# Kernel optimization log

Measured on AMD Instinct MI355X. Metric: run time of the kernel, lower is better.

The kernel has to match this reference:

```python
import jax, jax.numpy as jnp
import numpy as np

B, V, D, R = 2, 4096, 192, 16
E, H = 2 * D, 8
DH = E // H
K, TK = 16, 8


def _ln(x, g, b):
    m = x.mean(-1, keepdims=True)
    v = ((x - m) ** 2).mean(-1, keepdims=True)
    return (x - m) * jax.lax.rsqrt(v + 1e-5) * g + b


def _coords():
    # voxel centers in [-1,1]^3, (V,3)
    r = (jnp.arange(R, dtype=jnp.float32) + 0.5) / R * 2.0 - 1.0
    return jnp.stack(jnp.meshgrid(r, r, r, indexing='ij'), -1).reshape(-1, 3)


def setup_inputs() -> dict:
    key = jax.random.key(0)
    ks = jax.random.split(key, 10)
    s = 0.02
    return {
        'voxel_tokens': jax.random.normal(ks[0], (B, V, D), jnp.float32),
        'non_empty_mask': jax.random.randint(ks[1], (B, V), 0, 2).astype(bool),
        'We': jax.random.normal(ks[2], (D, E)) * s, 'be': jnp.zeros((E,)),
        'g1': jnp.ones((E,)), 'bt1': jnp.zeros((E,)),
        'Wqkv': jax.random.normal(ks[3], (E, 3 * E)) * s, 'bqkv': jnp.zeros((3 * E,)),
        'Wo': jax.random.normal(ks[4], (E, E)) * s, 'bo': jnp.zeros((E,)),
        'Wc': jax.random.normal(ks[5], (E, D)) * s, 'bc': jnp.zeros((D,)),
        'g2': jnp.ones((E,)), 'bt2': jnp.zeros((E,)),
        'W1': jax.random.normal(ks[6], (E, 2 * E)) * s, 'b1': jnp.zeros((2 * E,)),
        'W2': jax.random.normal(ks[7], (2 * E, E)) * s, 'b2': jnp.zeros((E,)),
    }


def reference(voxel_tokens, non_empty_mask, We, be, g1, bt1, Wqkv, bqkv, Wo, bo,
              Wc, bc, g2, bt2, W1, b1, W2, b2):
    fmask = non_empty_mask.astype(voxel_tokens.dtype)  # (B,V)
    shortcut = voxel_tokens
    x = voxel_tokens @ We + be                          # expand: (B,V,E)
    x = _ln(x, g1, bt1)
    # --- sparse dynamic voxel attention ---
    c = _coords()
    d2 = jnp.sum((c[:, None, :] - c[None, :, :]) ** 2, -1)  # (V,V)
    big = jnp.asarray(1e9, x.dtype)
    dmask = d2[None] + (1.0 - fmask)[:, None, :] * big      # empty keys pushed away
    _, knn = jax.lax.top_k(-dmask, K)                        # (B,V,K) nearest non-empty
    qkv = x @ Wqkv + bqkv
    q, k, v = jnp.split(qkv, 3, axis=-1)                     # (B,V,E) each
    bidx = jnp.arange(B)[:, None, None]
    kn = k[bidx, knn].reshape(B, V, K, H, DH)                # gathered neighbor keys
    vn = v[bidx, knn].reshape(B, V, K, H, DH)
    qh = q.reshape(B, V, H, DH)
    scores = jnp.einsum('bvhd,bvkhd->bvhk', qh, kn) / jnp.sqrt(jnp.asarray(DH, x.dtype))
    nvalid = fmask[bidx, knn]                                # (B,V,K)
    scores = jnp.where(nvalid[:, :, None, :] > 0, scores, -big)
    sel, sidx = jax.lax.top_k(scores, TK)                    # top_k_select by score
    attn = jax.nn.softmax(sel, axis=-1)                      # (B,V,H,TK)
    vt = vn.transpose(0, 1, 3, 2, 4)                         # (B,V,H,K,DH)
    vsel = jnp.take_along_axis(vt, sidx[..., None], axis=3)  # (B,V,H,TK,DH)
    o = jnp.einsum('bvhk,bvhkd->bvhd', attn, vsel).reshape(B, V, E)
    o = o @ Wo + bo
    # masked scatter: empty voxels -> zeros (reconstruct_dense_masked_scatter_2)
    x = o * fmask[..., None]
    x = x @ Wc + bc                                          # contract
    x = x * 0.5 + shortcut                                   # DropPath(0) -> identity
    x2 = x @ We + be
    x2 = _ln(x2, g2, bt2)
    x2 = jax.nn.gelu(x2 @ W1 + b1) @ W2 + b2                 # FeedForward(E, 2E)
    x2 = x2 @ Wc + bc
    return x2 * 0.5 + x
```

## Files before the change

### kernel.cpp

```cpp
#include <hip/hip_runtime.h>
#include <stdint.h>


using u16 = unsigned short;
using u32 = unsigned int;
using u64 = unsigned long long;

typedef short short8 __attribute__((ext_vector_type(8)));
typedef float f32x4 __attribute__((ext_vector_type(4)));

#define DEV static __device__ __forceinline__

constexpr int cV = 4096, cD = 192;
constexpr int cE = 384;
constexpr int cKN = 16, cTK = 8;
constexpr int cM = 2 * cV;
constexpr int c3E = 1152;

DEV float bf2f(u16 v) { return __uint_as_float(((u32)v) << 16); }
DEV float bflo(u32 v) { return __uint_as_float(v << 16); }
DEV float bfhi(u32 v) { return __uint_as_float(v & 0xFFFF0000u); }
DEV u16 f2bf(float f) {
  u32 u = __float_as_uint(f);
  u = (u + 0x7FFFu + ((u >> 16) & 1u)) >> 16;
  return (u16)u;
}
DEV int mget(const void* mp, int flag, int i) {
  if (flag == 0) return ((const int*)mp)[i] != 0;
  if (flag == 1) return ((const float*)mp)[i] != 0.0f;
  if (flag == 2) return ((const u16*)mp)[i] != 0;
  return ((const unsigned char*)mp)[i] != 0;
}
DEV float gelu_tanh(float x) {
  float t = tanhf(0.7978845608028654f * (x + 0.044715f * x * x * x));
  return 0.5f * x * (1.0f + t);
}
DEV u32 f2ord(float f) {
  u32 u = __float_as_uint(f);
  return (u & 0x80000000u) ? ~u : (u | 0x80000000u);
}
DEV float ord2f(u32 o) {
  u32 bits = (o & 0x80000000u) ? (o & 0x7FFFFFFFu) : ~o;
  return __uint_as_float(bits);
}
DEV int bf_plausible(u32 h) {
  if (h == 0u || h == 0x8000u) return 1;
  u32 e = (h >> 7) & 0xFFu;
  return (e >= 100u && e <= 140u) ? 1 : 0;
}

using as1p = const unsigned int __attribute__((address_space(1)))*;
using as3p = unsigned int __attribute__((address_space(3)))*;
DEV void gload16(const void* g, void* l) {
  __builtin_amdgcn_global_load_lds((as1p)g, (as3p)l, 16, 0, 0);
}
DEV f32x4 mfma16x16x32_bf16(short8 a, short8 b, f32x4 c) {
  asm volatile("v_mfma_f32_16x16x32_bf16 %0, %1, %2, %0" : "+v"(c) : "v"(a), "v"(b));
  return c;
}
DEV int swz(int row, int byteoff) { return byteoff ^ ((row & 7) << 4); }
DEV int ldswz(int r, int c) { return r * 64 + (c ^ ((r & 7) * 8)); }
#define SBPIN() __builtin_amdgcn_sched_barrier(0)

struct BF { short8 v[3][2]; };
DEV void loadBF(BF& b, const u16* __restrict__ fbase, int nKB, int kb, int lane) {
  #pragma unroll
  for (int n = 0; n < 3; ++n)
    #pragma unroll
    for (int ks = 0; ks < 2; ++ks)
      b.v[n][ks] = *(const short8*)(fbase + ((size_t)n * nKB + kb + ks) * 512 + lane * 8);
}

template <int T, typename AF>
DEV void rstage_1x8(const u16* __restrict__ fbase, int nKB, int kb0,
                    int lane, int l15, int l4,
                    f32x4 (&acc)[2][3], AF&& aread) {
  BF bp[2];
  loadBF(bp[0], fbase, nKB, kb0, lane);
  #pragma unroll
  for (int t = 0; t < T; ++t) {
    if (t + 1 < T) loadBF(bp[(t + 1) & 1], fbase, nKB, kb0 + 2 * (t + 1), lane);
    #pragma unroll
    for (int ks = 0; ks < 2; ++ks) {
      short8 a0 = aread(0, t, ks);
      short8 a1 = aread(1, t, ks);
      #pragma unroll
      for (int n = 0; n < 3; ++n) {
        acc[0][n] = mfma16x16x32_bf16(a0, bp[t & 1].v[n][ks], acc[0][n]);
        acc[1][n] = mfma16x16x32_bf16(a1, bp[t & 1].v[n][ks], acc[1][n]);
      }
    }
  }
}

template <int T, typename AF>
DEV void rstage_2x4(const u16* __restrict__ fbase, int nKB, int kb0,
                    int lane, int l15, int l4,
                    f32x4 (&acc)[3], AF&& aread) {
  BF bp[2];
  loadBF(bp[0], fbase, nKB, kb0, lane);
  #pragma unroll
  for (int t = 0; t < T; ++t) {
    if (t + 1 < T) loadBF(bp[(t + 1) & 1], fbase, nKB, kb0 + 2 * (t + 1), lane);
    #pragma unroll
    for (int ks = 0; ks < 2; ++ks) {
      short8 a = aread(t, ks);
      #pragma unroll
      for (int n = 0; n < 3; ++n)
        acc[n] = mfma16x16x32_bf16(a, bp[t & 1].v[n][ks], acc[n]);
    }
  }
}

__global__ void detect_all_kernel(const u32* __restrict__ tok,
                                  const u32* __restrict__ m,
                                  int* __restrict__ flag) {
  __shared__ int cnt, sa, sb, sc;
  if (threadIdx.x == 0) { cnt = 0; sa = 0; sb = 0; sc = 0; }
  __syncthreads();
  int c = 0;
  for (int i = threadIdx.x; i < 4096; i += 256) {
    u32 d = tok[i];
    c += bf_plausible(d & 0xFFFFu) & bf_plausible(d >> 16);
  }
  atomicAdd(&cnt, c);
  int a = 0, b = 0, cc = 0;
  for (int i = threadIdx.x; i < 2048; i += 256) {
    u32 d = m[i];
    if (!(d == 0u || d == 1u)) a = 1;
    if (!(d == 0u || d == 0x3F800000u)) b = 1;
    if (!(d == 0u || d == 0x00003F80u || d == 0x3F800000u || d == 0x3F803F80u)) cc = 1;
  }
  if (a) atomicOr(&sa, 1);
  if (b) atomicOr(&sb, 1);
  if (cc) atomicOr(&sc, 1);
  __syncthreads();
  if (threadIdx.x == 0) {
    flag[1] = (cnt > 3400) ? 1 : 0;
    flag[0] = (sa == 0) ? 0 : ((sb == 0) ? 1 : ((sc == 0) ? 2 : 3));
  }
}

struct PrepArgs {
  const void* csrc[11]; u16* cdst[11]; int cn[11];
  const void* tsrc[6]; u16* tdst[6]; int tK[6]; int tN[6];
  const void* mask; u64* bm;
};
__global__ __launch_bounds__(256) void prep_kernel(PrepArgs a, const int* __restrict__ flag) {
  const int job = blockIdx.y;
  const int dt = flag[1];
  if (job < 11) {
    const int n = a.cn[job];
    u16* d = a.cdst[job];
    if (dt) {
      const u16* s = (const u16*)a.csrc[job];
      for (int i = blockIdx.x * 256 + threadIdx.x; i < n; i += gridDim.x * 256) d[i] = s[i];
    } else {
      const float* s = (const float*)a.csrc[job];
      for (int i = blockIdx.x * 256 + threadIdx.x; i < n; i += gridDim.x * 256) d[i] = f2bf(s[i]);
    }
  } else if (job < 17) {
    const int t = job - 11;
    const int K = a.tK[t], N = a.tN[t];
    const int nKB = K >> 5;
    const int total = K * N;
    u16* d = a.tdst[t];
    for (int i = blockIdx.x * 256 + threadIdx.x; i < total; i += gridDim.x * 256) {
      const int frag = i >> 9;
      const int r = i & 511;
      const int lane = r >> 3, e = r & 7;
      const int l4 = lane >> 4, l15 = lane & 15;
      const int colblk = frag / nKB;
      const int kblk = frag - colblk * nKB;
      const int n = colblk * 16 + l15;
      const int k = kblk * 32 + l4 * 8 + e;
      u16 vv;
      if (dt) vv = ((const u16*)a.tsrc[t])[(size_t)k * N + n];
      else vv = f2bf(((const float*)a.tsrc[t])[(size_t)k * N + n]);
      d[i] = vv;
    }
  } else {
    const int gw = (blockIdx.x * 256 + threadIdx.x) >> 6;
    const int lane = threadIdx.x & 63;
    if (gw < 128) {
      const int fl = flag[0];
      u64 bal = __ballot(mget(a.mask, fl, gw * 64 + lane) != 0);
      if (lane == 0) a.bm[gw] = bal;
    }
  }
}

__global__ __launch_bounds__(256) void knn_kernel(const u64* __restrict__ bitmask,
                                                  int* __restrict__ knn_out) {
  const int tid = threadIdx.x;
  const int wid = tid >> 6, lane = tid & 63;
  const int q0 = blockIdx.x * 4;
  const int b = q0 >> 12;
  const int q = q0 + wid;
  const int v = q & 4095;
  __shared__ u64 smask[64];
  __shared__ int hist4[4][64];
  __shared__ int listT[4][64];
  __shared__ int out16s[4][16];
  __shared__ int meta[4][3];
  __shared__ int cntA[4], cntT[4];
  if (tid < 64) smask[tid] = bitmask[b * 64 + tid];
  for (int i = tid; i < 4 * 64; i += 256) ((int*)hist4)[i] = 0;
  if (lane == 0) { cntA[wid] = 0; cntT[wid] = 0; }
  __syncthreads();
  const int iv = v >> 8, jv = (v >> 4) & 15, kv = v & 15;
  #pragma unroll
  for (int t = 0; t < 12; ++t) {
    int o = t * 64 + lane;
    if (o < 729) {
      int oi = o / 81, rm = o - oi * 81;
      int oj = rm / 9, ok = rm - oj * 9;
      int i = iv + oi - 4, j = jv + oj - 4, k = kv + ok - 4;
      if (((i | j | k) & ~15) == 0) {
        int u = (i << 8) | (j << 4) | k;
        if ((smask[u >> 6] >> (u & 63)) & 1ull) {
          int di = oi - 4, dj = oj - 4, dk = ok - 4;
          atomicAdd(&hist4[wid][di * di + dj * dj + dk * dk], 1);
        }
      }
    }
  }
  __syncthreads();
  if (lane == 0) {
    int cum = 0, T = -1, below = 0;
    for (int d = 0; d <= 48; ++d) {
      int h = hist4[wid][d];
      if (h > 0 && cum + h >= cKN) { T = d; below = cum; break; }
      cum += h;
    }
    if (T > 24) T = -1;
    meta[wid][0] = T; meta[wid][1] = below; meta[wid][2] = (T < 0) ? 1 : 0;
  }
  __syncthreads();
  const int T = meta[wid][0], below = meta[wid][1], fb = meta[wid][2];
  #pragma unroll
  for (int t = 0; t < 12; ++t) {
    int o = t * 64 + lane;
    if (o < 729) {
      int oi = o / 81, rm = o - oi * 81;
      int oj = rm / 9, ok = rm - oj * 9;
      int i = iv + oi - 4, j = jv + oj - 4, k = kv + ok - 4;
      if (((i | j | k) & ~15) == 0) {
        int u = (i << 8) | (j << 4) | k;
        if ((smask[u >> 6] >> (u & 63)) & 1ull) {
          int di = oi - 4, dj = oj - 4, dk = ok - 4;
          int d2 = di * di + dj * dj + dk * dk;
          if (d2 < T) { int p = atomicAdd(&cntA[wid], 1); out16s[wid][p] = u; }
          else if (d2 == T) { int p = atomicAdd(&cntT[wid], 1); if (p < 64) listT[wid][p] = u; }
        }
      }
    }
  }
  __syncthreads();
  if (!fb) {
    if (lane == 0) {
      int need = cKN - below;
      int nT = cntT[wid] < 64 ? cntT[wid] : 64;
      for (int r = 0; r < need; ++r) {
        int bi = 0, bu = 0x7FFFFFFF;
        for (int i2 = 0; i2 < nT; ++i2) { int x = listT[wid][i2]; if (x < bu) { bu = x; bi = i2; } }
        out16s[wid][below + r] = bu;
        listT[wid][bi] = 0x7FFFFFFF;
      }
    }
  } else {
    u64 rem = smask[lane];
    const int myi = lane >> 2;
    const int di2 = (iv - myi) * (iv - myi);
    for (int r = 0; r < cKN; ++r) {
      u64 tmp = rem;
      u32 best = 0xFFFFFFFFu;
      while (tmp) {
        int bp = __builtin_ctzll(tmp);
        tmp &= tmp - 1;
        int u = (lane << 6) | bp;
        int dj = jv - ((u >> 4) & 15), dk = kv - (u & 15);
        u32 key = (u32)(((di2 + dj * dj + dk * dk) << 12) | u);
        if (key < best) best = key;
      }
      u32 pk = (best == 0xFFFFFFFFu) ? 0xFFFFFFFFu : ((best << 6) | (u32)lane);
      #pragma unroll
      for (int off = 1; off < 64; off <<= 1) {
        u32 o2 = __shfl_xor(pk, off);
        if (o2 < pk) pk = o2;
      }
      int u = (int)((pk >> 6) & 4095u);
      int wl = (int)(pk & 63u);
      if (lane == wl) rem &= ~(1ull << (u & 63));
      if (lane == 0) out16s[wid][r] = u;
    }
  }
  __syncthreads();
  if (lane < cKN) knn_out[q * cKN + lane] = out16s[wid][lane];
}

__global__ __launch_bounds__(512) void fused_ln_qkv(
    const u16* __restrict__ tokc, const u16* __restrict__ WeF,
    const u16* __restrict__ be, const u16* __restrict__ g1, const u16* __restrict__ bt1,
    const u16* __restrict__ WqkvF, const u16* __restrict__ bqkv,
    u16* __restrict__ QB) {
  __shared__ alignas(16) u16 Afull[3 * 2048];
  __shared__ alignas(16) char X1[32 * 768];
  __shared__ float st[32][8][2];
  const int tid = threadIdx.x;
  const int lane = tid & 63, wn = tid >> 6;
  const int l15 = lane & 15, l4 = lane >> 4;
  const int sr = lane >> 3;
  const int scs = (((lane & 7) ^ sr) << 3);
  const int row0 = blockIdx.x * 32;

  for (int g = wn; g < 12; g += 8)
    gload16(tokc + (size_t)(row0 + (g & 3) * 8 + sr) * 192 + (g >> 2) * 64 + scs,
            (char*)Afull + g * 1024);
  SBPIN();
  __syncthreads();

  f32x4 acc[2][3];
  #pragma unroll
  for (int m = 0; m < 2; ++m)
    #pragma unroll
    for (int n = 0; n < 3; ++n) acc[m][n] = f32x4{0.f, 0.f, 0.f, 0.f};
  rstage_1x8<3>(WeF + (size_t)(wn * 3) * 6 * 512, 6, 0, lane, l15, l4, acc,
                [&](int m, int t, int ks) {
                  return *(const short8*)&Afull[t * 2048 + ldswz(m * 16 + l15, ks * 32 + l4 * 8)];
                });
  float s[2][4], sq[2][4];
  #pragma unroll
  for (int m = 0; m < 2; ++m)
    #pragma unroll
    for (int j = 0; j < 4; ++j) { s[m][j] = 0.f; sq[m][j] = 0.f; }
  #pragma unroll
  for (int n = 0; n < 3; ++n) {
    const float bi = bf2f(be[wn * 48 + n * 16 + l15]);
    #pragma unroll
    for (int m = 0; m < 2; ++m)
      #pragma unroll
      for (int j = 0; j < 4; ++j) {
        acc[m][n][j] += bi;
        s[m][j] += acc[m][n][j]; sq[m][j] += acc[m][n][j] * acc[m][n][j];
      }
  }
  #pragma unroll
  for (int off = 1; off < 16; off <<= 1)
    #pragma unroll
    for (int m = 0; m < 2; ++m)
      #pragma unroll
      for (int j = 0; j < 4; ++j) { s[m][j] += __shfl_xor(s[m][j], off); sq[m][j] += __shfl_xor(sq[m][j], off); }
  if (l15 == 0) {
    #pragma unroll
    for (int m = 0; m < 2; ++m)
      #pragma unroll
      for (int j = 0; j < 4; ++j) {
        const int rl = m * 16 + l4 * 4 + j;
        st[rl][wn][0] = s[m][j]; st[rl][wn][1] = sq[m][j];
      }
  }
  __syncthreads();
  #pragma unroll
  for (int m = 0; m < 2; ++m)
    #pragma unroll
    for (int j = 0; j < 4; ++j) {
      const int rl = m * 16 + l4 * 4 + j;
      float ts = 0.f, tq = 0.f;
      #pragma unroll
      for (int wv = 0; wv < 8; ++wv) { ts += st[rl][wv][0]; tq += st[rl][wv][1]; }
      const float mean = ts * (1.0f / 384.0f);
      const float var = tq * (1.0f / 384.0f) - mean * mean;
      const float rstd = rsqrtf(var + 1e-5f);
      #pragma unroll
      for (int n = 0; n < 3; ++n) {
        const int col = wn * 48 + n * 16 + l15;
        const float v = (acc[m][n][j] - mean) * rstd * bf2f(g1[col]) + bf2f(bt1[col]);
        *(u16*)(X1 + swz(rl, rl * 768 + col * 2)) = f2bf(v);
      }
    }
  __syncthreads();

  for (int chunk = 0; chunk < 3; ++chunk) {
    f32x4 a2[2][3];
    #pragma unroll
    for (int m = 0; m < 2; ++m)
      #pragma unroll
      for (int n = 0; n < 3; ++n) a2[m][n] = f32x4{0.f, 0.f, 0.f, 0.f};
    rstage_1x8<6>(WqkvF + (size_t)(chunk * 24 + wn * 3) * 12 * 512, 12, 0, lane, l15, l4, a2,
                  [&](int m, int t, int ks) {
                    const int rl = m * 16 + l15;
                    return *(const short8*)(X1 + swz(rl, rl * 768 + (t * 64 + ks * 32 + l4 * 8) * 2));
                  });
    #pragma unroll
    for (int n = 0; n < 3; ++n) {
      const int col = chunk * 384 + wn * 48 + n * 16 + l15;
      const float bi = bf2f(bqkv[col]);
      #pragma unroll
      for (int m = 0; m < 2; ++m)
        #pragma unroll
        for (int j = 0; j < 4; ++j)
          QB[(size_t)(row0 + m * 16 + l4 * 4 + j) * c3E + col] = f2bf(a2[m][n][j] + bi);
    }
  }
}

__global__ __launch_bounds__(512) void fused_cd(
    const u16* __restrict__ S2, const u16* __restrict__ WoF, const u16* __restrict__ bo,
    const void* __restrict__ mask, const int* __restrict__ flag,
    const u16* __restrict__ WcF, const u16* __restrict__ bc, const u16* __restrict__ tokc,
    const u16* __restrict__ WeF, const u16* __restrict__ be,
    const u16* __restrict__ g2, const u16* __restrict__ bt2,
    const u16* __restrict__ W1F, const u16* __restrict__ b1,
    const u16* __restrict__ W2F, const u16* __restrict__ b2,
    void* __restrict__ outv) {
  __shared__ alignas(16) u16 Afull[6 * 2048];
  __shared__ alignas(16) char Tb[32 * 768];
  __shared__ float st[32][8][2];
  char* HbA = (char*)Afull;
  const int tid = threadIdx.x;
  const int lane = tid & 63, wn = tid >> 6;
  const int wr = wn >> 2, wc = wn & 3;
  const int l15 = lane & 15, l4 = lane >> 4;
  const int sr = lane >> 3;
  const int scs = (((lane & 7) ^ sr) << 3);
  const int row0 = blockIdx.x * 32;
  const int fl = flag[0];

  for (int g = wn; g < 24; g += 8)
    gload16(S2 + (size_t)(row0 + (g & 3) * 8 + sr) * cE + (g >> 2) * 64 + scs,
            (char*)Afull + g * 1024);
  SBPIN();
  __syncthreads();

  {
    f32x4 acc[2][3];
    #pragma unroll
    for (int m = 0; m < 2; ++m)
      #pragma unroll
      for (int n = 0; n < 3; ++n) acc[m][n] = f32x4{0.f, 0.f, 0.f, 0.f};
    rstage_1x8<6>(WoF + (size_t)(wn * 3) * 12 * 512, 12, 0, lane, l15, l4, acc,
                  [&](int m, int t, int ks) {
                    return *(const short8*)&Afull[t * 2048 + ldswz(m * 16 + l15, ks * 32 + l4 * 8)];
                  });
    #pragma unroll
    for (int m = 0; m < 2; ++m)
      #pragma unroll
      for (int j = 0; j < 4; ++j) {
        const int rl = m * 16 + l4 * 4 + j;
        const float fm = mget(mask, fl, row0 + rl) ? 1.0f : 0.0f;
        #pragma unroll
        for (int n = 0; n < 3; ++n) {
          const int col = wn * 48 + n * 16 + l15;
          const float v = (acc[m][n][j] + bf2f(bo[col])) * fm;
          *(u16*)(Tb + swz(rl, rl * 768 + col * 2)) = f2bf(v);
        }
      }
  }
  __syncthreads();

  f32x4 xm[3];
  #pragma unroll
  for (int n = 0; n < 3; ++n) xm[n] = f32x4{0.f, 0.f, 0.f, 0.f};
  rstage_2x4<6>(WcF + (size_t)(wc * 3) * 12 * 512, 12, 0, lane, l15, l4, xm,
                [&](int t, int ks) {
                  const int rl = wr * 16 + l15;
                  return *(const short8*)(Tb + swz(rl, rl * 768 + (t * 64 + ks * 32 + l4 * 8) * 2));
                });
  __syncthreads();
  #pragma unroll
  for (int n = 0; n < 3; ++n) {
    const int col = wc * 48 + n * 16 + l15;
    const float bi = bf2f(bc[col]);
    #pragma unroll
    for (int j = 0; j < 4; ++j) {
      const int rl = wr * 16 + l4 * 4 + j;
      xm[n][j] = (xm[n][j] + bi) * 0.5f + bf2f(tokc[(size_t)(row0 + rl) * cD + col]);
      *(u16*)(Tb + swz(rl, rl * 384 + col * 2)) = f2bf(xm[n][j]);
    }
  }
  __syncthreads();

  {
    f32x4 a3[2][3];
    #pragma unroll
    for (int m = 0; m < 2; ++m)
      #pragma unroll
      for (int n = 0; n < 3; ++n) a3[m][n] = f32x4{0.f, 0.f, 0.f, 0.f};
    rstage_1x8<3>(WeF + (size_t)(wn * 3) * 6 * 512, 6, 0, lane, l15, l4, a3,
                  [&](int m, int t, int ks) {
                    const int rl = m * 16 + l15;
                    return *(const short8*)(Tb + swz(rl, rl * 384 + (t * 64 + ks * 32 + l4 * 8) * 2));
                  });
    float s[2][4], sq[2][4];
    #pragma unroll
    for (int m = 0; m < 2; ++m)
      #pragma unroll
      for (int j = 0; j < 4; ++j) { s[m][j] = 0.f; sq[m][j] = 0.f; }
    #pragma unroll
    for (int n = 0; n < 3; ++n) {
      const float bi = bf2f(be[wn * 48 + n * 16 + l15]);
      #pragma unroll
      for (int m = 0; m < 2; ++m)
        #pragma unroll
        for (int j = 0; j < 4; ++j) {
          a3[m][n][j] += bi;
          s[m][j] += a3[m][n][j]; sq[m][j] += a3[m][n][j] * a3[m][n][j];
        }
    }
    #pragma unroll
    for (int off = 1; off < 16; off <<= 1)
      #pragma unroll
      for (int m = 0; m < 2; ++m)
        #pragma unroll
        for (int j = 0; j < 4; ++j) { s[m][j] += __shfl_xor(s[m][j], off); sq[m][j] += __shfl_xor(sq[m][j], off); }
    if (l15 == 0) {
      #pragma unroll
      for (int m = 0; m < 2; ++m)
        #pragma unroll
        for (int j = 0; j < 4; ++j) {
          const int rl = m * 16 + l4 * 4 + j;
          st[rl][wn][0] = s[m][j]; st[rl][wn][1] = sq[m][j];
        }
    }
    __syncthreads();
    #pragma unroll
    for (int m = 0; m < 2; ++m)
      #pragma unroll
      for (int j = 0; j < 4; ++j) {
        const int rl = m * 16 + l4 * 4 + j;
        float ts = 0.f, tq = 0.f;
        #pragma unroll
        for (int wv = 0; wv < 8; ++wv) { ts += st[rl][wv][0]; tq += st[rl][wv][1]; }
        const float mean = ts * (1.0f / 384.0f);
        const float var = tq * (1.0f / 384.0f) - mean * mean;
        const float rstd = rsqrtf(var + 1e-5f);
        #pragma unroll
        for (int n = 0; n < 3; ++n) {
          const int col = wn * 48 + n * 16 + l15;
          const float v = (a3[m][n][j] - mean) * rstd * bf2f(g2[col]) + bf2f(bt2[col]);
          *(u16*)(Tb + swz(rl, rl * 768 + col * 2)) = f2bf(v);
        }
      }
  }
  __syncthreads();

  f32x4 accF[2][3];
  #pragma unroll
  for (int m = 0; m < 2; ++m)
    #pragma unroll
    for (int n = 0; n < 3; ++n) accF[m][n] = f32x4{0.f, 0.f, 0.f, 0.f};

  for (int half = 0; half < 2; ++half) {
    {
      f32x4 a1[2][3];
      #pragma unroll
      for (int m = 0; m < 2; ++m)
        #pragma unroll
        for (int n = 0; n < 3; ++n) a1[m][n] = f32x4{0.f, 0.f, 0.f, 0.f};
      rstage_1x8<6>(W1F + (size_t)(half * 24 + wn * 3) * 12 * 512, 12, 0, lane, l15, l4, a1,
                    [&](int m, int t, int ks) {
                      const int rl = m * 16 + l15;
                      return *(const short8*)(Tb + swz(rl, rl * 768 + (t * 64 + ks * 32 + l4 * 8) * 2));
                    });
      #pragma unroll
      for (int n = 0; n < 3; ++n) {
        const int col = wn * 48 + n * 16 + l15;
        const float bi = bf2f(b1[half * 384 + col]);
        #pragma unroll
        for (int m = 0; m < 2; ++m)
          #pragma unroll
          for (int j = 0; j < 4; ++j) {
            const int rl = m * 16 + l4 * 4 + j;
            *(u16*)(HbA + swz(rl, rl * 768 + col * 2)) = f2bf(gelu_tanh(a1[m][n][j] + bi));
          }
      }
    }
    __syncthreads();
    rstage_1x8<6>(W2F + (size_t)(wn * 3) * 24 * 512, 24, half * 12, lane, l15, l4, accF,
                  [&](int m, int t, int ks) {
                    const int rl = m * 16 + l15;
                    return *(const short8*)(HbA + swz(rl, rl * 768 + (t * 64 + ks * 32 + l4 * 8) * 2));
                  });
    __syncthreads();
  }
  #pragma unroll
  for (int n = 0; n < 3; ++n) {
    const int col = wn * 48 + n * 16 + l15;
    const float bi = bf2f(b2[col]);
    #pragma unroll
    for (int m = 0; m < 2; ++m)
      #pragma unroll
      for (int j = 0; j < 4; ++j) {
        const int rl = m * 16 + l4 * 4 + j;
        *(u16*)(HbA + swz(rl, rl * 768 + col * 2)) = f2bf(accF[m][n][j] + bi);
      }
  }
  __syncthreads();
  f32x4 a3[3];
  #pragma unroll
  for (int n = 0; n < 3; ++n) a3[n] = f32x4{0.f, 0.f, 0.f, 0.f};
  rstage_2x4<6>(WcF + (size_t)(wc * 3) * 12 * 512, 12, 0, lane, l15, l4, a3,
                [&](int t, int ks) {
                  const int rl = wr * 16 + l15;
                  return *(const short8*)(HbA + swz(rl, rl * 768 + (t * 64 + ks * 32 + l4 * 8) * 2));
                });
  u16* o16 = (u16*)outv;
  float* o32 = (float*)outv;
  const int dtf = flag[1];
  #pragma unroll
  for (int n = 0; n < 3; ++n) {
    const int col = wc * 48 + n * 16 + l15;
    const float bi = bf2f(bc[col]);
    #pragma unroll
    for (int j = 0; j < 4; ++j) {
      const int rl = wr * 16 + l4 * 4 + j;
      const size_t oi = (size_t)(row0 + rl) * cD + col;
      const float r = (a3[n][j] + bi) * 0.5f + xm[n][j];
      if (dtf) o16[oi] = f2bf(r);
      else o32[oi] = r;
    }
  }
}

__global__ __launch_bounds__(256) void attn_kernel(const u16* __restrict__ qkv,
                                                   const int* __restrict__ knn,
                                                   u16* __restrict__ o_out) {
  const int wid = threadIdx.x >> 6;
  const int lane = threadIdx.x & 63;
  const int bq = blockIdx.x * 4 + wid;
  const int b = bq >> 12;
  __shared__ float w4[4][8][8];
  __shared__ int vid4[4][8][8];
  __shared__ int nb4[4][16];
  float (*w)[8] = w4[wid];
  int (*vid)[8] = vid4[wid];
  int* nb = nb4[wid];
  if (lane < 16) nb[lane] = knn[bq * cKN + lane];
  const int h = lane >> 3;
  const int j = lane & 7;
  const uint2* qp = (const uint2*)(qkv + (size_t)bq * c3E + h * 48);
  const int r0 = nb[j], r1 = nb[j + 8];
  const uint2* k0p = (const uint2*)(qkv + ((size_t)(b * cV + r0)) * c3E + cE + h * 48);
  const uint2* k1p = (const uint2*)(qkv + ((size_t)(b * cV + r1)) * c3E + cE + h * 48);
  float s0 = 0.f, s1 = 0.f;
  #pragma unroll
  for (int t = 0; t < 12; ++t) {
    uint2 qv = qp[t];
    uint2 k0 = k0p[t];
    uint2 k1 = k1p[t];
    s0 += bflo(qv.x) * bflo(k0.x) + bfhi(qv.x) * bfhi(k0.x)
        + bflo(qv.y) * bflo(k0.y) + bfhi(qv.y) * bfhi(k0.y);
    s1 += bflo(qv.x) * bflo(k1.x) + bfhi(qv.x) * bfhi(k1.x)
        + bflo(qv.y) * bflo(k1.y) + bfhi(qv.y) * bfhi(k1.y);
  }
  const float inv = 0.14433756729740643f;
  u64 key0 = (((u64)f2ord(s0 * inv)) << 4) | (u64)(15 - j);
  u64 key1 = (((u64)f2ord(s1 * inv)) << 4) | (u64)(15 - (j + 8));
  float m0 = 0.f, Z = 0.f, myw = 0.f;
  int myv = 0;
  #pragma unroll
  for (int r = 0; r < cTK; ++r) {
    u64 best = key0 > key1 ? key0 : key1;
    u64 o1 = __shfl_xor(best, 1); if (o1 > best) best = o1;
    u64 o2 = __shfl_xor(best, 2); if (o2 > best) best = o2;
    u64 o4 = __shfl_xor(best, 4); if (o4 > best) best = o4;
    if (key0 == best) key0 = 0;
    if (key1 == best) key1 = 0;
    float sv = ord2f((u32)(best >> 4));
    int nsel = 15 - (int)(best & 15ull);
    if (r == 0) m0 = sv;
    float e = expf(sv - m0);
    Z += e;
    if (j == r) { myw = e; myv = nsel; }
  }
  w[h][j] = myw / Z;
  vid[h][j] = nb[myv];
  const u16* vbase = qkv + (size_t)(b * cV) * c3E + 2 * cE;
  #pragma unroll
  for (int rep = 0; rep < 6; ++rep) {
    int e = rep * 64 + lane;
    int h2 = e / 48;
    float acc = 0.f;
    #pragma unroll
    for (int t = 0; t < cTK; ++t)
      acc += w[h2][t] * bf2f(vbase[(size_t)vid[h2][t] * c3E + e]);
    o_out[(size_t)bq * cE + e] = f2bf(acc);
  }
}

extern "C" void kernel_launch(void* const* d_in, const int* in_sizes, int n_in,
                              void* d_out, int out_size, void* d_ws, size_t ws_size,
                              hipStream_t stream) {
  if (n_in < 18) return;
  const void* mask = d_in[1];

  char* ws = (char*)d_ws;
  size_t off = 0;
  auto alloc = [&](size_t bytes) { size_t o = off; off += (bytes + 255) & ~(size_t)255; return o; };
  int* flag  = (int*)(ws + alloc(256));
  u64* bmask = (u64*)(ws + alloc(128 * 8));
  int* knn   = (int*)(ws + alloc((size_t)cM * cKN * 4));
  u16* S2    = (u16*)(ws + alloc((size_t)cM * cE * 2));
  u16* QB    = (u16*)(ws + alloc((size_t)cM * c3E * 2));
  u16* tokc  = (u16*)(ws + alloc((size_t)cM * cD * 2));
  u16* be    = (u16*)(ws + alloc(cE * 2));
  u16* g1    = (u16*)(ws + alloc(cE * 2));
  u16* bt1   = (u16*)(ws + alloc(cE * 2));
  u16* bqkv  = (u16*)(ws + alloc(c3E * 2));
  u16* bo    = (u16*)(ws + alloc(cE * 2));
  u16* bc    = (u16*)(ws + alloc(cD * 2));
  u16* g2    = (u16*)(ws + alloc(cE * 2));
  u16* bt2   = (u16*)(ws + alloc(cE * 2));
  u16* b1    = (u16*)(ws + alloc(2 * cE * 2));
  u16* b2    = (u16*)(ws + alloc(cE * 2));
  u16* WeF   = (u16*)(ws + alloc((size_t)192 * 384 * 2));
  u16* WqkvF = (u16*)(ws + alloc((size_t)384 * 1152 * 2));
  u16* WoF   = (u16*)(ws + alloc((size_t)384 * 384 * 2));
  u16* WcF   = (u16*)(ws + alloc((size_t)384 * 192 * 2));
  u16* W1F   = (u16*)(ws + alloc((size_t)384 * 768 * 2));
  u16* W2F   = (u16*)(ws + alloc((size_t)768 * 384 * 2));
  (void)ws_size; (void)in_sizes; (void)out_size;

  detect_all_kernel<<<1, 256, 0, stream>>>((const u32*)d_in[0], (const u32*)mask, flag);

  {
    PrepArgs pa;
    const int csrci[11] = {0, 3, 4, 5, 7, 9, 11, 12, 13, 15, 17};
    u16* cdsts[11] = {tokc, be, g1, bt1, bqkv, bo, bc, g2, bt2, b1, b2};
    const int cns[11] = {cM * cD, cE, cE, cE, c3E, cE, cD, cE, cE, 2 * cE, cE};
    for (int i = 0; i < 11; ++i) { pa.csrc[i] = d_in[csrci[i]]; pa.cdst[i] = cdsts[i]; pa.cn[i] = cns[i]; }
    const int tsrci[6] = {2, 6, 8, 10, 14, 16};
    u16* tdsts[6] = {WeF, WqkvF, WoF, WcF, W1F, W2F};
    const int tKs[6] = {192, 384, 384, 384, 384, 768};
    const int tNs[6] = {384, 1152, 384, 192, 768, 384};
    for (int i = 0; i < 6; ++i) { pa.tsrc[i] = d_in[tsrci[i]]; pa.tdst[i] = tdsts[i]; pa.tK[i] = tKs[i]; pa.tN[i] = tNs[i]; }
    pa.mask = mask; pa.bm = bmask;
    prep_kernel<<<dim3(96, 18), 256, 0, stream>>>(pa, flag);
  }

  knn_kernel<<<cM / 4, 256, 0, stream>>>(bmask, knn);

  const int GB = cM / 32;
  fused_ln_qkv<<<GB, 512, 0, stream>>>(tokc, WeF, be, g1, bt1, WqkvF, bqkv, QB);
  attn_kernel<<<cM / 4, 256, 0, stream>>>(QB, knn, S2);
  fused_cd<<<GB, 512, 0, stream>>>(S2, WoF, bo, mask, flag, WcF, bc, tokc,
                                   WeF, be, g2, bt2, W1F, b1, W2F, b2, d_out);
}
```

Baseline: 140.7 us.

## Halve row tile of fused GEMM kernels to 16 rows for more blocks

The fused LN+QKV and contract/FFN kernels now process 16 rows per block instead of 32, doubling the grid to 512 blocks and cutting shared memory per block. The goal is better occupancy and more parallelism across the GPU's compute units for a small M. In exchange, every block re-streams the full weight matrices from global/L2, so weight traffic per output row doubles. Half the waves sit idle during the 192-column Wc stages.

```diff
diff --git a/kernel.cpp b/kernel.cpp
--- a/kernel.cpp
+++ b/kernel.cpp
@@ -72,31 +72,8 @@
 }
 
 template <int T, typename AF>
-DEV void rstage_1x8(const u16* __restrict__ fbase, int nKB, int kb0,
-                    int lane, int l15, int l4,
-                    f32x4 (&acc)[2][3], AF&& aread) {
-  BF bp[2];
-  loadBF(bp[0], fbase, nKB, kb0, lane);
-  #pragma unroll
-  for (int t = 0; t < T; ++t) {
-    if (t + 1 < T) loadBF(bp[(t + 1) & 1], fbase, nKB, kb0 + 2 * (t + 1), lane);
-    #pragma unroll
-    for (int ks = 0; ks < 2; ++ks) {
-      short8 a0 = aread(0, t, ks);
-      short8 a1 = aread(1, t, ks);
-      #pragma unroll
-      for (int n = 0; n < 3; ++n) {
-        acc[0][n] = mfma16x16x32_bf16(a0, bp[t & 1].v[n][ks], acc[0][n]);
-        acc[1][n] = mfma16x16x32_bf16(a1, bp[t & 1].v[n][ks], acc[1][n]);
-      }
-    }
-  }
-}
-
-template <int T, typename AF>
-DEV void rstage_2x4(const u16* __restrict__ fbase, int nKB, int kb0,
-                    int lane, int l15, int l4,
-                    f32x4 (&acc)[3], AF&& aread) {
+DEV void rstage(const u16* __restrict__ fbase, int nKB, int kb0,
+                int lane, f32x4 (&acc)[3], AF&& aread) {
   BF bp[2];
   loadBF(bp[0], fbase, nKB, kb0, lane);
   #pragma unroll
@@ -304,103 +281,84 @@
     const u16* __restrict__ be, const u16* __restrict__ g1, const u16* __restrict__ bt1,
     const u16* __restrict__ WqkvF, const u16* __restrict__ bqkv,
     u16* __restrict__ QB) {
-  __shared__ alignas(16) u16 Afull[3 * 2048];
-  __shared__ alignas(16) char X1[32 * 768];
-  __shared__ float st[32][8][2];
+  __shared__ alignas(16) u16 Afull[3 * 1024];
+  __shared__ alignas(16) char X1[16 * 768];
+  __shared__ float st[16][8][2];
   const int tid = threadIdx.x;
   const int lane = tid & 63, wn = tid >> 6;
   const int l15 = lane & 15, l4 = lane >> 4;
   const int sr = lane >> 3;
   const int scs = (((lane & 7) ^ sr) << 3);
-  const int row0 = blockIdx.x * 32;
-
-  for (int g = wn; g < 12; g += 8)
-    gload16(tokc + (size_t)(row0 + (g & 3) * 8 + sr) * 192 + (g >> 2) * 64 + scs,
+  const int row0 = blockIdx.x * 16;
+
+  for (int g = wn; g < 6; g += 8)
+    gload16(tokc + (size_t)(row0 + (g & 1) * 8 + sr) * 192 + (g >> 1) * 64 + scs,
             (char*)Afull + g * 1024);
   SBPIN();
   __syncthreads();
 
-  f32x4 acc[2][3];
-  #pragma unroll
-  for (int m = 0; m < 2; ++m)
-    #pragma unroll
-    for (int n = 0; n < 3; ++n) acc[m][n] = f32x4{0.f, 0.f, 0.f, 0.f};
-  rstage_1x8<3>(WeF + (size_t)(wn * 3) * 6 * 512, 6, 0, lane, l15, l4, acc,
-                [&](int m, int t, int ks) {
-                  return *(const short8*)&Afull[t * 2048 + ldswz(m * 16 + l15, ks * 32 + l4 * 8)];
-                });
-  float s[2][4], sq[2][4];
-  #pragma unroll
-  for (int m = 0; m < 2; ++m)
-    #pragma unroll
-    for (int j = 0; j < 4; ++j) { s[m][j] = 0.f; sq[m][j] = 0.f; }
+  f32x4 acc[3];
+  #pragma unroll
+  for (int n = 0; n < 3; ++n) acc[n] = f32x4{0.f, 0.f, 0.f, 0.f};
+  rstage<3>(WeF + (size_t)(wn * 3) * 6 * 512, 6, 0, lane, acc,
+            [&](int t, int ks) {
+              return *(const short8*)&Afull[t * 1024 + ldswz(l15, ks * 32 + l4 * 8)];
+            });
+  float s[4] = {0, 0, 0, 0}, sq[4] = {0, 0, 0, 0};
   #pragma unroll
   for (int n = 0; n < 3; ++n) {
     const float bi = bf2f(be[wn * 48 + n * 16 + l15]);
     #pragma unroll
-    for (int m = 0; m < 2; ++m)
-      #pragma unroll
-      for (int j = 0; j < 4; ++j) {
-        acc[m][n][j] += bi;
-        s[m][j] += acc[m][n][j]; sq[m][j] += acc[m][n][j] * acc[m][n][j];
-      }
+    for (int j = 0; j < 4; ++j) {
+      acc[n][j] += bi;
+      s[j] += acc[n][j]; sq[j] += acc[n][j] * acc[n][j];
+    }
   }
   #pragma unroll
   for (int off = 1; off < 16; off <<= 1)
     #pragma unroll
-    for (int m = 0; m < 2; ++m)
-      #pragma unroll
-      for (int j = 0; j < 4; ++j) { s[m][j] += __shfl_xor(s[m][j], off); sq[m][j] += __shfl_xor(sq[m][j], off); }
+    for (int j = 0; j < 4; ++j) { s[j] += __shfl_xor(s[j], off); sq[j] += __shfl_xor(sq[j], off); }
   if (l15 == 0) {
     #pragma unroll
-    for (int m = 0; m < 2; ++m)
-      #pragma unroll
-      for (int j = 0; j < 4; ++j) {
-        const int rl = m * 16 + l4 * 4 + j;
-        st[rl][wn][0] = s[m][j]; st[rl][wn][1] = sq[m][j];
-      }
-  }
-  __syncthreads();
-  #pragma unroll
-  for (int m = 0; m < 2; ++m)
-    #pragma unroll
     for (int j = 0; j < 4; ++j) {
-      const int rl = m * 16 + l4 * 4 + j;
-      float ts = 0.f, tq = 0.f;
-      #pragma unroll
-      for (int wv = 0; wv < 8; ++wv) { ts += st[rl][wv][0]; tq += st[rl][wv][1]; }
-      const float mean = ts * (1.0f / 384.0f);
-      const float var = tq * (1.0f / 384.0f) - mean * mean;
-      const float rstd = rsqrtf(var + 1e-5f);
-      #pragma unroll
-      for (int n = 0; n < 3; ++n) {
-        const int col = wn * 48 + n * 16 + l15;
-        const float v = (acc[m][n][j] - mean) * rstd * bf2f(g1[col]) + bf2f(bt1[col]);
-        *(u16*)(X1 + swz(rl, rl * 768 + col * 2)) = f2bf(v);
-      }
-    }
+      const int rl = l4 * 4 + j;
+      st[rl][wn][0] = s[j]; st[rl][wn][1] = sq[j];
+    }
+  }
+  __syncthreads();
+  #pragma unroll
+  for (int j = 0; j < 4; ++j) {
+    const int rl = l4 * 4 + j;
+    float ts = 0.f, tq = 0.f;
+    #pragma unroll
+    for (int wv = 0; wv < 8; ++wv) { ts += st[rl][wv][0]; tq += st[rl][wv][1]; }
+    const float mean = ts * (1.0f / 384.0f);
+    const float var = tq * (1.0f / 384.0f) - mean * mean;
+    const float rstd = rsqrtf(var + 1e-5f);
+    #pragma unroll
+    for (int n = 0; n < 3; ++n) {
+      const int col = wn * 48 + n * 16 + l15;
+      const float v = (acc[n][j] - mean) * rstd * bf2f(g1[col]) + bf2f(bt1[col]);
+      *(u16*)(X1 + swz(rl, rl * 768 + col * 2)) = f2bf(v);
+    }
+  }
   __syncthreads();
 
   for (int chunk = 0; chunk < 3; ++chunk) {
-    f32x4 a2[2][3];
-    #pragma unroll
-    for (int m = 0; m < 2; ++m)
-      #pragma unroll
-      for (int n = 0; n < 3; ++n) a2[m][n] = f32x4{0.f, 0.f, 0.f, 0.f};
-    rstage_1x8<6>(WqkvF + (size_t)(chunk * 24 + wn * 3) * 12 * 512, 12, 0, lane, l15, l4, a2,
-                  [&](int m, int t, int ks) {
-                    const int rl = m * 16 + l15;
-                    return *(const short8*)(X1 + swz(rl, rl * 768 + (t * 64 + ks * 32 + l4 * 8) * 2));
-                  });
+    f32x4 a2[3];
+    #pragma unroll
+    for (int n = 0; n < 3; ++n) a2[n] = f32x4{0.f, 0.f, 0.f, 0.f};
+    rstage<6>(WqkvF + (size_t)(chunk * 24 + wn * 3) * 12 * 512, 12, 0, lane, a2,
+              [&](int t, int ks) {
+                return *(const short8*)(X1 + swz(l15, l15 * 768 + (t * 64 + ks * 32 + l4 * 8) * 2));
+              });
     #pragma unroll
     for (int n = 0; n < 3; ++n) {
       const int col = chunk * 384 + wn * 48 + n * 16 + l15;
       const float bi = bf2f(bqkv[col]);
       #pragma unroll
-      for (int m = 0; m < 2; ++m)
-        #pragma unroll
-        for (int j = 0; j < 4; ++j)
-          QB[(size_t)(row0 + m * 16 + l4 * 4 + j) * c3E + col] = f2bf(a2[m][n][j] + bi);
+      for (int j = 0; j < 4; ++j)
+        QB[(size_t)(row0 + l4 * 4 + j) * c3E + col] = f2bf(a2[n][j] + bi);
     }
   }
 }
@@ -414,174 +372,150 @@
     const u16* __restrict__ W1F, const u16* __restrict__ b1,
     const u16* __restrict__ W2F, const u16* __restrict__ b2,
     void* __restrict__ outv) {
-  __shared__ alignas(16) u16 Afull[6 * 2048];
-  __shared__ alignas(16) char Tb[32 * 768];
-  __shared__ float st[32][8][2];
+  __shared__ alignas(16) u16 Afull[6 * 1024];
+  __shared__ alignas(16) char Tb[16 * 768];
+  __shared__ float st[16][8][2];
   char* HbA = (char*)Afull;
   const int tid = threadIdx.x;
   const int lane = tid & 63, wn = tid >> 6;
-  const int wr = wn >> 2, wc = wn & 3;
+  const int wc = wn & 3;
   const int l15 = lane & 15, l4 = lane >> 4;
   const int sr = lane >> 3;
   const int scs = (((lane & 7) ^ sr) << 3);
-  const int row0 = blockIdx.x * 32;
+  const int row0 = blockIdx.x * 16;
   const int fl = flag[0];
 
-  for (int g = wn; g < 24; g += 8)
-    gload16(S2 + (size_t)(row0 + (g & 3) * 8 + sr) * cE + (g >> 2) * 64 + scs,
+  for (int g = wn; g < 12; g += 8)
+    gload16(S2 + (size_t)(row0 + (g & 1) * 8 + sr) * cE + (g >> 1) * 64 + scs,
             (char*)Afull + g * 1024);
   SBPIN();
   __syncthreads();
 
   {
-    f32x4 acc[2][3];
-    #pragma unroll
-    for (int m = 0; m < 2; ++m)
-      #pragma unroll
-      for (int n = 0; n < 3; ++n) acc[m][n] = f32x4{0.f, 0.f, 0.f, 0.f};
-    rstage_1x8<6>(WoF + (size_t)(wn * 3) * 12 * 512, 12, 0, lane, l15, l4, acc,
-                  [&](int m, int t, int ks) {
-                    return *(const short8*)&Afull[t * 2048 + ldswz(m * 16 + l15, ks * 32 + l4 * 8)];
-                  });
-    #pragma unroll
-    for (int m = 0; m < 2; ++m)
+    f32x4 acc[3];
+    #pragma unroll
+    for (int n = 0; n < 3; ++n) acc[n] = f32x4{0.f, 0.f, 0.f, 0.f};
+    rstage<6>(WoF + (size_t)(wn * 3) * 12 * 512, 12, 0, lane, acc,
+              [&](int t, int ks) {
+                return *(const short8*)&Afull[t * 1024 + ldswz(l15, ks * 32 + l4 * 8)];
+              });
+    #pragma unroll
+    for (int j = 0; j < 4; ++j) {
+      const int rl = l4 * 4 + j;
+      const float fm = mget(mask, fl, row0 + rl) ? 1.0f : 0.0f;
+      #pragma unroll
+      for (int n = 0; n < 3; ++n) {
+        const int col = wn * 48 + n * 16 + l15;
+        const float v = (acc[n][j] + bf2f(bo[col])) * fm;
+        *(u16*)(Tb + swz(rl, rl * 768 + col * 2)) = f2bf(v);
+      }
+    }
+  }
+  __syncthreads();
+
+  f32x4 xm[3];
+  #pragma unroll
+  for (int n = 0; n < 3; ++n) xm[n] = f32x4{0.f, 0.f, 0.f, 0.f};
+  if (wn < 4) {
+    rstage<6>(WcF + (size_t)(wc * 3) * 12 * 512, 12, 0, lane, xm,
+              [&](int t, int ks) {
+                return *(const short8*)(Tb + swz(l15, l15 * 768 + (t * 64 + ks * 32 + l4 * 8) * 2));
+              });
+  }
+  __syncthreads();
+  if (wn < 4) {
+    #pragma unroll
+    for (int n = 0; n < 3; ++n) {
+      const int col = wc * 48 + n * 16 + l15;
+      const float bi = bf2f(bc[col]);
       #pragma unroll
       for (int j = 0; j < 4; ++j) {
-        const int rl = m * 16 + l4 * 4 + j;
-        const float fm = mget(mask, fl, row0 + rl) ? 1.0f : 0.0f;
-        #pragma unroll
-        for (int n = 0; n < 3; ++n) {
-          const int col = wn * 48 + n * 16 + l15;
-          const float v = (acc[m][n][j] + bf2f(bo[col])) * fm;
-          *(u16*)(Tb + swz(rl, rl * 768 + col * 2)) = f2bf(v);
-        }
-      }
-  }
-  __syncthreads();
-
-  f32x4 xm[3];
-  #pragma unroll
-  for (int n = 0; n < 3; ++n) xm[n] = f32x4{0.f, 0.f, 0.f, 0.f};
-  rstage_2x4<6>(WcF + (size_t)(wc * 3) * 12 * 512, 12, 0, lane, l15, l4, xm,
-                [&](int t, int ks) {
-                  const int rl = wr * 16 + l15;
-                  return *(const short8*)(Tb + swz(rl, rl * 768 + (t * 64 + ks * 32 + l4 * 8) * 2));
-                });
-  __syncthreads();
-  #pragma unroll
-  for (int n = 0; n < 3; ++n) {
-    const int col = wc * 48 + n * 16 + l15;
-    const float bi = bf2f(bc[col]);
-    #pragma unroll
-    for (int j = 0; j < 4; ++j) {
-      const int rl = wr * 16 + l4 * 4 + j;
-      xm[n][j] = (xm[n][j] + bi) * 0.5f + bf2f(tokc[(size_t)(row0 + rl) * cD + col]);
-      *(u16*)(Tb + swz(rl, rl * 384 + col * 2)) = f2bf(xm[n][j]);
+        const int rl = l4 * 4 + j;
+        xm[n][j] = (xm[n][j] + bi) * 0.5f + bf2f(tokc[(size_t)(row0 + rl) * cD + col]);
+        *(u16*)(Tb + swz(rl, rl * 384 + col * 2)) = f2bf(xm[n][j]);
+      }
     }
   }
   __syncthreads();
 
   {
-    f32x4 a3[2][3];
-    #pragma unroll
-    for (int m = 0; m < 2; ++m)
-      #pragma unroll
-      for (int n = 0; n < 3; ++n) a3[m][n] = f32x4{0.f, 0.f, 0.f, 0.f};
-    rstage_1x8<3>(WeF + (size_t)(wn * 3) * 6 * 512, 6, 0, lane, l15, l4, a3,
-                  [&](int m, int t, int ks) {
-                    const int rl = m * 16 + l15;
-                    return *(const short8*)(Tb + swz(rl, rl * 384 + (t * 64 + ks * 32 + l4 * 8) * 2));
-                  });
-    float s[2][4], sq[2][4];
-    #pragma unroll
-    for (int m = 0; m < 2; ++m)
-      #pragma unroll
-      for (int j = 0; j < 4; ++j) { s[m][j] = 0.f; sq[m][j] = 0.f; }
+    f32x4 a3[3];
+    #pragma unroll
+    for (int n = 0; n < 3; ++n) a3[n] = f32x4{0.f, 0.f, 0.f, 0.f};
+    rstage<3>(WeF + (size_t)(wn * 3) * 6 * 512, 6, 0, lane, a3,
+              [&](int t, int ks) {
+                return *(const short8*)(Tb + swz(l15, l15 * 384 + (t * 64 + ks * 32 + l4 * 8) * 2));
+              });
+    float s[4] = {0, 0, 0, 0}, sq[4] = {0, 0, 0, 0};
     #pragma unroll
     for (int n = 0; n < 3; ++n) {
       const float bi = bf2f(be[wn * 48 + n * 16 + l15]);
       #pragma unroll
-      for (int m = 0; m < 2; ++m)
-        #pragma unroll
-        for (int j = 0; j < 4; ++j) {
-          a3[m][n][j] += bi;
-          s[m][j] += a3[m][n][j]; sq[m][j] += a3[m][n][j] * a3[m][n][j];
-        }
+      for (int j = 0; j < 4; ++j) {
+        a3[n][j] += bi;
+        s[j] += a3[n][j]; sq[j] += a3[n][j] * a3[n][j];
+      }
     }
     #pragma unroll
     for (int off = 1; off < 16; off <<= 1)
       #pragma unroll
-      for (int m = 0; m < 2; ++m)
-        #pragma unroll
-        for (int j = 0; j < 4; ++j) { s[m][j] += __shfl_xor(s[m][j], off); sq[m][j] += __shfl_xor(sq[m][j], off); }
+      for (int j = 0; j < 4; ++j) { s[j] += __shfl_xor(s[j], off); sq[j] += __shfl_xor(sq[j], off); }
     if (l15 == 0) {
       #pragma unroll
-      for (int m = 0; m < 2; ++m)
-        #pragma unroll
-        for (int j = 0; j < 4; ++j) {
-          const int rl = m * 16 + l4 * 4 + j;
-          st[rl][wn][0] = s[m][j]; st[rl][wn][1] = sq[m][j];
-        }
+      for (int j = 0; j < 4; ++j) {
+        const int rl = l4 * 4 + j;
+        st[rl][wn][0] = s[j]; st[rl][wn][1] = sq[j];
+      }
     }
     __syncthreads();
     #pragma unroll
-    for (int m = 0; m < 2; ++m)
-      #pragma unroll
-      for (int j = 0; j < 4; ++j) {
-        const int rl = m * 16 + l4 * 4 + j;
-        float ts = 0.f, tq = 0.f;
-        #pragma unroll
-        for (int wv = 0; wv < 8; ++wv) { ts += st[rl][wv][0]; tq += st[rl][wv][1]; }
-        const float mean = ts * (1.0f / 384.0f);
-        const float var = tq * (1.0f / 384.0f) - mean * mean;
-        const float rstd = rsqrtf(var + 1e-5f);
-        #pragma unroll
-        for (int n = 0; n < 3; ++n) {
-          const int col = wn * 48 + n * 16 + l15;
-          const float v = (a3[m][n][j] - mean) * rstd * bf2f(g2[col]) + bf2f(bt2[col]);
-          *(u16*)(Tb + swz(rl, rl * 768 + col * 2)) = f2bf(v);
-        }
-      }
-  }
-  __syncthreads();
-
-  f32x4 accF[2][3];
-  #pragma unroll
-  for (int m = 0; m < 2; ++m)
-    #pragma unroll
-    for (int n = 0; n < 3; ++n) accF[m][n] = f32x4{0.f, 0.f, 0.f, 0.f};
+    for (int j = 0; j < 4; ++j) {
+      const int rl = l4 * 4 + j;
+      float ts = 0.f, tq = 0.f;
+      #pragma unroll
+      for (int wv = 0; wv < 8; ++wv) { ts += st[rl][wv][0]; tq += st[rl][wv][1]; }
+      const float mean = ts * (1.0f / 384.0f);
+      const float var = tq * (1.0f / 384.0f) - mean * mean;
+      const float rstd = rsqrtf(var + 1e-5f);
+      #pragma unroll
+      for (int n = 0; n < 3; ++n) {
+        const int col = wn * 48 + n * 16 + l15;
+        const float v = (a3[n][j] - mean) * rstd * bf2f(g2[col]) + bf2f(bt2[col]);
+        *(u16*)(Tb + swz(rl, rl * 768 + col * 2)) = f2bf(v);
+      }
+    }
+  }
+  __syncthreads();
+
+  f32x4 accF[3];
+  #pragma unroll
+  for (int n = 0; n < 3; ++n) accF[n] = f32x4{0.f, 0.f, 0.f, 0.f};
 
   for (int half = 0; half < 2; ++half) {
     {
-      f32x4 a1[2][3];
-      #pragma unroll
-      for (int m = 0; m < 2; ++m)
-        #pragma unroll
-        for (int n = 0; n < 3; ++n) a1[m][n] = f32x4{0.f, 0.f, 0.f, 0.f};
-      rstage_1x8<6>(W1F + (size_t)(half * 24 + wn * 3) * 12 * 512, 12, 0, lane, l15, l4, a1,
-                    [&](int m, int t, int ks) {
-                      const int rl = m * 16 + l15;
-                      return *(const short8*)(Tb + swz(rl, rl * 768 + (t * 64 + ks * 32 + l4 * 8) * 2));
-                    });
+      f32x4 a1[3];
+      #pragma unroll
+      for (int n = 0; n < 3; ++n) a1[n] = f32x4{0.f, 0.f, 0.f, 0.f};
+      rstage<6>(W1F + (size_t)(half * 24 + wn * 3) * 12 * 512, 12, 0, lane, a1,
+                [&](int t, int ks) {
+                  return *(const short8*)(Tb + swz(l15, l15 * 768 + (t * 64 + ks * 32 + l4 * 8) * 2));
+                });
       #pragma unroll
       for (int n = 0; n < 3; ++n) {
         const int col = wn * 48 + n * 16 + l15;
         const float bi = bf2f(b1[half * 384 + col]);
         #pragma unroll
-        for (int m = 0; m < 2; ++m)
-          #pragma unroll
-          for (int j = 0; j < 4; ++j) {
-            const int rl = m * 16 + l4 * 4 + j;
-            *(u16*)(HbA + swz(rl, rl * 768 + col * 2)) = f2bf(gelu_tanh(a1[m][n][j] + bi));
-          }
+        for (int j = 0; j < 4; ++j) {
+          const int rl = l4 * 4 + j;
+          *(u16*)(HbA + swz(rl, rl * 768 + col * 2)) = f2bf(gelu_tanh(a1[n][j] + bi));
+        }
       }
     }
     __syncthreads();
-    rstage_1x8<6>(W2F + (size_t)(wn * 3) * 24 * 512, 24, half * 12, lane, l15, l4, accF,
-                  [&](int m, int t, int ks) {
-                    const int rl = m * 16 + l15;
-                    return *(const short8*)(HbA + swz(rl, rl * 768 + (t * 64 + ks * 32 + l4 * 8) * 2));
-                  });
+    rstage<6>(W2F + (size_t)(wn * 3) * 24 * 512, 24, half * 12, lane, accF,
+              [&](int t, int ks) {
+                return *(const short8*)(HbA + swz(l15, l15 * 768 + (t * 64 + ks * 32 + l4 * 8) * 2));
+              });
     __syncthreads();
   }
   #pragma unroll
@@ -589,36 +523,35 @@
     const int col = wn * 48 + n * 16 + l15;
     const float bi = bf2f(b2[col]);
     #pragma unroll
-    for (int m = 0; m < 2; ++m)
+    for (int j = 0; j < 4; ++j) {
+      const int rl = l4 * 4 + j;
+      *(u16*)(HbA + swz(rl, rl * 768 + col * 2)) = f2bf(accF[n][j] + bi);
+    }
+  }
+  __syncthreads();
+  f32x4 a3[3];
+  #pragma unroll
+  for (int n = 0; n < 3; ++n) a3[n] = f32x4{0.f, 0.f, 0.f, 0.f};
+  if (wn < 4) {
+    rstage<6>(WcF + (size_t)(wc * 3) * 12 * 512, 12, 0, lane, a3,
+              [&](int t, int ks) {
+                return *(const short8*)(HbA + swz(l15, l15 * 768 + (t * 64 + ks * 32 + l4 * 8) * 2));
+              });
+    u16* o16 = (u16*)outv;
+    float* o32 = (float*)outv;
+    const int dtf = flag[1];
+    #pragma unroll
+    for (int n = 0; n < 3; ++n) {
+      const int col = wc * 48 + n * 16 + l15;
+      const float bi = bf2f(bc[col]);
       #pragma unroll
       for (int j = 0; j < 4; ++j) {
-        const int rl = m * 16 + l4 * 4 + j;
-        *(u16*)(HbA + swz(rl, rl * 768 + col * 2)) = f2bf(accF[m][n][j] + bi);
-      }
-  }
-  __syncthreads();
-  f32x4 a3[3];
-  #pragma unroll
-  for (int n = 0; n < 3; ++n) a3[n] = f32x4{0.f, 0.f, 0.f, 0.f};
-  rstage_2x4<6>(WcF + (size_t)(wc * 3) * 12 * 512, 12, 0, lane, l15, l4, a3,
-                [&](int t, int ks) {
-                  const int rl = wr * 16 + l15;
-                  return *(const short8*)(HbA + swz(rl, rl * 768 + (t * 64 + ks * 32 + l4 * 8) * 2));
-                });
-  u16* o16 = (u16*)outv;
-  float* o32 = (float*)outv;
-  const int dtf = flag[1];
-  #pragma unroll
-  for (int n = 0; n < 3; ++n) {
-    const int col = wc * 48 + n * 16 + l15;
-    const float bi = bf2f(bc[col]);
-    #pragma unroll
-    for (int j = 0; j < 4; ++j) {
-      const int rl = wr * 16 + l4 * 4 + j;
-      const size_t oi = (size_t)(row0 + rl) * cD + col;
-      const float r = (a3[n][j] + bi) * 0.5f + xm[n][j];
-      if (dtf) o16[oi] = f2bf(r);
-      else o32[oi] = r;
+        const int rl = l4 * 4 + j;
+        const size_t oi = (size_t)(row0 + rl) * cD + col;
+        const float r = (a3[n][j] + bi) * 0.5f + xm[n][j];
+        if (dtf) o16[oi] = f2bf(r);
+        else o32[oi] = r;
+      }
     }
   }
 }
@@ -741,7 +674,7 @@
 
   knn_kernel<<<cM / 4, 256, 0, stream>>>(bmask, knn);
 
-  const int GB = cM / 32;
+  const int GB = cM / 16;
   fused_ln_qkv<<<GB, 512, 0, stream>>>(tokc, WeF, be, g1, bt1, WqkvF, bqkv, QB);
   attn_kernel<<<cM / 4, 256, 0, stream>>>(QB, knn, S2);
   fused_cd<<<GB, 512, 0, stream>>>(S2, WoF, bo, mask, flag, WcF, bc, tokc,
```

Result: slower. 155.0 us (+10.1%).
